# Kernel optimization log

Hardware: AMD Instinct MI355X
Metric: run time of the kernel (lower is better)

The kernel has to match this reference:

```python
import jax, jax.numpy as jnp
import numpy as np

D_MODEL, D_STATE, D_CONV, EXPAND = 1024, 16, 4, 2
D_INNER = EXPAND * D_MODEL
BATCH, SEQLEN = 2, 1024


def setup_inputs() -> dict:
    key = jax.random.key(0)
    ks = jax.random.split(key, 8)
    s = lambda fan: 1.0 / np.sqrt(fan)
    x = jax.random.normal(ks[0], (BATCH, SEQLEN, D_MODEL), jnp.float32)
    in_proj_w = jax.random.normal(ks[1], (2 * D_INNER, D_MODEL), jnp.float32) * s(D_MODEL)
    conv_w = jax.random.normal(ks[2], (D_INNER, D_CONV), jnp.float32) * s(D_CONV)
    conv_b = jax.random.normal(ks[3], (D_INNER,), jnp.float32) * 0.02
    x_proj_w = jax.random.normal(ks[4], (2 * D_STATE + 1, D_INNER), jnp.float32) * s(D_INNER)
    dt_proj_w = jax.random.normal(ks[5], (D_INNER, 1), jnp.float32)
    dt_proj_b = jax.random.normal(ks[6], (D_INNER,), jnp.float32) * 0.02
    A_log = jnp.log(jnp.broadcast_to(jnp.arange(1, D_STATE + 1, dtype=jnp.float32), (D_INNER, D_STATE)))
    D_param = jnp.ones((D_INNER,), jnp.float32)
    out_proj_w = jax.random.normal(ks[7], (D_MODEL, D_INNER), jnp.float32) * s(D_INNER)
    return {"x": x, "in_proj_w": in_proj_w, "conv_w": conv_w, "conv_b": conv_b,
            "x_proj_w": x_proj_w, "dt_proj_w": dt_proj_w, "dt_proj_b": dt_proj_b,
            "A_log": A_log, "D_param": D_param, "out_proj_w": out_proj_w}


def reference(x, in_proj_w, conv_w, conv_b, x_proj_w, dt_proj_w, dt_proj_b, A_log, D_param, out_proj_w):
    B, L, _ = x.shape
    d_inner, d_conv = conv_w.shape
    N = A_log.shape[1]

    # in_proj: [B,L,d_model] -> [B,L,2*d_inner], split into ssm branch and gate
    xz = x @ in_proj_w.T
    x_ssm, z = jnp.split(xz, 2, axis=-1)

    # causal depthwise conv1d (padding d_conv-1 on the left, truncated to L)
    xpad = jnp.pad(x_ssm, ((0, 0), (d_conv - 1, 0), (0, 0)))
    xc = conv_b + sum(conv_w[:, k] * xpad[:, k:k + L, :] for k in range(d_conv))
    xc = jax.nn.silu(xc)

    # selective SSM
    A = -jnp.exp(A_log)                                    # [d_inner, N]
    xp = xc @ x_proj_w.T                                   # [B,L,2N+1]
    dt_r, Bv, Cv = xp[..., :1], xp[..., 1:1 + N], xp[..., 1 + N:]
    dt = jax.nn.softplus(dt_r @ dt_proj_w.T + dt_proj_b)   # [B,L,d_inner]
    dA = jnp.exp(dt[..., None] * A)                        # [B,L,d_inner,N]
    dBx = (dt * xc)[..., None] * Bv[:, :, None, :]         # [B,L,d_inner,N]

    def step(h, inputs):
        dA_t, dBx_t, C_t = inputs                          # [B,D,N],[B,D,N],[B,N]
        h = dA_t * h + dBx_t
        y = jnp.einsum('bdn,bn->bd', h, C_t)
        return h, y

    h0 = jnp.zeros((B, d_inner, N), x.dtype)
    xs = (jnp.moveaxis(dA, 1, 0), jnp.moveaxis(dBx, 1, 0), jnp.moveaxis(Cv, 1, 0))
    _, ys = jax.lax.scan(step, h0, xs)                     # ys: [L,B,d_inner]
    y = jnp.moveaxis(ys, 0, 1) + xc * D_param

    y = y * jax.nn.silu(z)
    return y @ out_proj_w.T
```

## Files before the change

kernel.cpp:

```cpp
#include <hip/hip_runtime.h>
#include <hip/hip_bf16.h>
#include <math.h>

#define B_   2
#define L_   1024
#define DM   1024
#define DI   2048
#define NS   16
#define NPJ  33
#define XPW_STRIDE 64
#define NCH  32
#define CHL  32

typedef __bf16 bf16x8 __attribute__((ext_vector_type(8)));
typedef float  f32x4  __attribute__((ext_vector_type(4)));

__device__ __forceinline__ unsigned short f2bf_rn(float x) {
    union { float f; unsigned u; } a; a.f = x;
    unsigned r = a.u + 0x7fffu + ((a.u >> 16) & 1u);
    return (unsigned short)(r >> 16);
}
__device__ __forceinline__ float bf2f(unsigned short h) {
    union { unsigned u; float f; } a; a.u = ((unsigned)h) << 16;
    return a.f;
}
__device__ __forceinline__ float sigmoidf_(float x) { return 1.f / (1.f + __expf(-x)); }
__device__ __forceinline__ float softplusf_(float x) {
    return x > 20.f ? x : log1pf(__expf(x));
}

#define GLDS(g, l) __builtin_amdgcn_global_load_lds( \
    (__attribute__((address_space(1))) void*)(g),    \
    (__attribute__((address_space(3))) void*)(l), 16, 0, 0)

__global__ __launch_bounds__(256) void cast_hilo_kernel(
    const float* __restrict__ in, unsigned short* __restrict__ hi,
    unsigned short* __restrict__ lo, int n4)
{
    int i = blockIdx.x * 256 + threadIdx.x;
    if (i >= n4) return;
    float4 v = ((const float4*)in)[i];
    ushort4 H, L;
    H.x = f2bf_rn(v.x); L.x = f2bf_rn(v.x - bf2f(H.x));
    H.y = f2bf_rn(v.y); L.y = f2bf_rn(v.y - bf2f(H.y));
    H.z = f2bf_rn(v.z); L.z = f2bf_rn(v.z - bf2f(H.z));
    H.w = f2bf_rn(v.w); L.w = f2bf_rn(v.w - bf2f(H.w));
    ((ushort4*)hi)[i] = H;
    ((ushort4*)lo)[i] = L;
}

__global__ __launch_bounds__(256) void cast_pad_w_kernel(
    const float* __restrict__ W, unsigned short* __restrict__ wh,
    unsigned short* __restrict__ wl)
{
    int i = blockIdx.x * 256 + threadIdx.x;
    int j = i >> 9;
    float4 v = make_float4(0.f, 0.f, 0.f, 0.f);
    if (j < NPJ) v = ((const float4*)W)[i];
    ushort4 H, L;
    H.x = f2bf_rn(v.x); L.x = f2bf_rn(v.x - bf2f(H.x));
    H.y = f2bf_rn(v.y); L.y = f2bf_rn(v.y - bf2f(H.y));
    H.z = f2bf_rn(v.z); L.z = f2bf_rn(v.z - bf2f(H.z));
    H.w = f2bf_rn(v.w); L.w = f2bf_rn(v.w - bf2f(H.w));
    ((ushort4*)wh)[i] = H;
    ((ushort4*)wl)[i] = L;
}

template<int BM, int BN, bool AL>
__global__ __launch_bounds__(256) void gemm3_bt(
    const unsigned short* __restrict__ Ah, const unsigned short* __restrict__ Al,
    const unsigned short* __restrict__ Bh, const unsigned short* __restrict__ Bl,
    float* __restrict__ C, int M, int N, int K, int KC)
{
    constexpr int BK = 64;
    constexpr int FM = BM / 32;
    constexpr int FN = BN / 32;
    __shared__ alignas(16) char sAh[BM * BK * 2];
    __shared__ alignas(16) char sAl[AL ? BM * BK * 2 : 16];
    __shared__ alignas(16) char sBh[BN * BK * 2];
    __shared__ alignas(16) char sBl[BN * BK * 2];

    const int tid  = threadIdx.x;
    const int lane = tid & 63;
    const int wave = tid >> 6;
    const int wm = wave >> 1, wn = wave & 1;
    const int m0 = blockIdx.y * BM, n0 = blockIdx.x * BN;
    const int k0 = blockIdx.z * KC;

    f32x4 acc[FM][FN];
#pragma unroll
    for (int i = 0; i < FM; ++i)
#pragma unroll
        for (int j = 0; j < FN; ++j)
            acc[i][j] = (f32x4){0.f, 0.f, 0.f, 0.f};

    for (int kt = k0; kt < k0 + KC; kt += BK) {
#pragma unroll
        for (int iss = 0; iss < BM / 32; ++iss) {
            int o  = (iss * 256 + tid) * 16;
            int r  = o >> 7;
            int cb = (o & 127) ^ ((r & 7) << 4);
            size_t goff = (size_t)(m0 + r) * K + kt + (cb >> 1);
            GLDS(Ah + goff, sAh + iss * 4096 + wave * 1024);
            if (AL) GLDS(Al + goff, sAl + iss * 4096 + wave * 1024);
        }
#pragma unroll
        for (int iss = 0; iss < BN / 32; ++iss) {
            int o  = (iss * 256 + tid) * 16;
            int r  = o >> 7;
            int cb = (o & 127) ^ ((r & 7) << 4);
            size_t goff = (size_t)(n0 + r) * K + kt + (cb >> 1);
            GLDS(Bh + goff, sBh + iss * 4096 + wave * 1024);
            GLDS(Bl + goff, sBl + iss * 4096 + wave * 1024);
        }
        __syncthreads();

#pragma unroll
        for (int kk = 0; kk < 2; ++kk) {
            const int ke = kk * 32 + (lane >> 4) * 8;
            bf16x8 ah[FM], al[FM], bh[FN], bl[FN];
#pragma unroll
            for (int i = 0; i < FM; ++i) {
                int r = wm * (BM / 2) + i * 16 + (lane & 15);
                int off = (r * 128 + ke * 2) ^ ((r & 7) << 4);
                ah[i] = *(const bf16x8*)(sAh + off);
                if (AL) al[i] = *(const bf16x8*)(sAl + off);
            }
#pragma unroll
            for (int j = 0; j < FN; ++j) {
                int r = wn * (BN / 2) + j * 16 + (lane & 15);
                int off = (r * 128 + ke * 2) ^ ((r & 7) << 4);
                bh[j] = *(const bf16x8*)(sBh + off);
                bl[j] = *(const bf16x8*)(sBl + off);
            }
#pragma unroll
            for (int i = 0; i < FM; ++i)
#pragma unroll
                for (int j = 0; j < FN; ++j) {
                    acc[i][j] = __builtin_amdgcn_mfma_f32_16x16x32_bf16(ah[i], bh[j], acc[i][j], 0, 0, 0);
                    acc[i][j] = __builtin_amdgcn_mfma_f32_16x16x32_bf16(ah[i], bl[j], acc[i][j], 0, 0, 0);
                    if (AL) acc[i][j] = __builtin_amdgcn_mfma_f32_16x16x32_bf16(al[i], bh[j], acc[i][j], 0, 0, 0);
                }
        }
        __syncthreads();
    }

    float* Cz = C + (size_t)blockIdx.z * M * N;
#pragma unroll
    for (int i = 0; i < FM; ++i)
#pragma unroll
        for (int j = 0; j < FN; ++j) {
            int row = m0 + wm * (BM / 2) + i * 16 + (lane >> 4) * 4;
            int col = n0 + wn * (BN / 2) + j * 16 + (lane & 15);
            float* p = Cz + (size_t)row * N + col;
#pragma unroll
            for (int q = 0; q < 4; ++q) p[(size_t)q * N] = acc[i][j][q];
        }
}

__global__ __launch_bounds__(256) void reduce4_kernel(
    const float* __restrict__ part, float* __restrict__ out, int n4, int stride4)
{
    int i = blockIdx.x * 256 + threadIdx.x;
    if (i >= n4) return;
    const float4* p = (const float4*)part;
    float4 s = p[i];
#pragma unroll
    for (int z = 1; z < 4; ++z) {
        float4 v = p[(size_t)z * stride4 + i];
        s.x += v.x; s.y += v.y; s.z += v.z; s.w += v.w;
    }
    ((float4*)out)[i] = s;
}

__global__ __launch_bounds__(256) void gemm3_xproj(
    const unsigned short* __restrict__ Ah, const unsigned short* __restrict__ Al,
    const unsigned short* __restrict__ Bh, const unsigned short* __restrict__ Bl,
    float* __restrict__ part)
{
    constexpr int BM = 64, BN = 64, BK = 64, KTOT = 2048, KC = 256;
    __shared__ alignas(16) char sAh[BM * 128];
    __shared__ alignas(16) char sAl[BM * 128];
    __shared__ alignas(16) char sBh[BN * 128];
    __shared__ alignas(16) char sBl[BN * 128];

    const int tid  = threadIdx.x;
    const int lane = tid & 63;
    const int wave = tid >> 6;
    const int wm = wave >> 1, wn = wave & 1;
    const int m0 = blockIdx.y * BM;
    const int kt0 = blockIdx.z * KC;

    f32x4 acc[2][2];
#pragma unroll
    for (int i = 0; i < 2; ++i)
#pragma unroll
        for (int j = 0; j < 2; ++j) acc[i][j] = (f32x4){0.f, 0.f, 0.f, 0.f};

    for (int kt = 0; kt < KC; kt += BK) {
#pragma unroll
        for (int iss = 0; iss < 2; ++iss) {
            int o  = (iss * 256 + tid) * 16;
            int r  = o >> 7;
            int cb = (o & 127) ^ ((r & 7) << 4);
            size_t ga = (size_t)(m0 + r) * KTOT + kt0 + kt + (cb >> 1);
            GLDS(Ah + ga, sAh + iss * 4096 + wave * 1024);
            GLDS(Al + ga, sAl + iss * 4096 + wave * 1024);
            size_t gb = (size_t)r * KTOT + kt0 + kt + (cb >> 1);
            GLDS(Bh + gb, sBh + iss * 4096 + wave * 1024);
            GLDS(Bl + gb, sBl + iss * 4096 + wave * 1024);
        }
        __syncthreads();

#pragma unroll
        for (int kk = 0; kk < 2; ++kk) {
            const int ke = kk * 32 + (lane >> 4) * 8;
            bf16x8 ah[2], al[2], bh[2], bl[2];
#pragma unroll
            for (int i = 0; i < 2; ++i) {
                int r = wm * 32 + i * 16 + (lane & 15);
                int off = (r * 128 + ke * 2) ^ ((r & 7) << 4);
                ah[i] = *(const bf16x8*)(sAh + off);
                al[i] = *(const bf16x8*)(sAl + off);
            }
#pragma unroll
            for (int j = 0; j < 2; ++j) {
                int r = wn * 32 + j * 16 + (lane & 15);
                int off = (r * 128 + ke * 2) ^ ((r & 7) << 4);
                bh[j] = *(const bf16x8*)(sBh + off);
                bl[j] = *(const bf16x8*)(sBl + off);
            }
#pragma unroll
            for (int i = 0; i < 2; ++i)
#pragma unroll
                for (int j = 0; j < 2; ++j) {
                    acc[i][j] = __builtin_amdgcn_mfma_f32_16x16x32_bf16(ah[i], bh[j], acc[i][j], 0, 0, 0);
                    acc[i][j] = __builtin_amdgcn_mfma_f32_16x16x32_bf16(ah[i], bl[j], acc[i][j], 0, 0, 0);
                    acc[i][j] = __builtin_amdgcn_mfma_f32_16x16x32_bf16(al[i], bh[j], acc[i][j], 0, 0, 0);
                }
        }
        __syncthreads();
    }

    float* Cp = part + (size_t)blockIdx.z * 2048 * XPW_STRIDE;
#pragma unroll
    for (int i = 0; i < 2; ++i)
#pragma unroll
        for (int j = 0; j < 2; ++j) {
            int row = m0 + wm * 32 + i * 16 + (lane >> 4) * 4;
            int col = wn * 32 + j * 16 + (lane & 15);
            float* p = Cp + (size_t)row * XPW_STRIDE + col;
#pragma unroll
            for (int q = 0; q < 4; ++q) p[(size_t)q * XPW_STRIDE] = acc[i][j][q];
        }
}

__global__ __launch_bounds__(256) void xproj_reduce(
    const float* __restrict__ part, float* __restrict__ xp)
{
    int i = blockIdx.x * 256 + threadIdx.x;
    const float4* p = (const float4*)part;
    float4 s = p[i];
#pragma unroll
    for (int z = 1; z < 8; ++z) {
        float4 v = p[(size_t)z * 32768 + i];
        s.x += v.x; s.y += v.y; s.z += v.z; s.w += v.w;
    }
    ((float4*)xp)[i] = s;
}

__global__ __launch_bounds__(256) void conv_silu_kernel(
    const float* __restrict__ xz, const float* __restrict__ cw,
    const float* __restrict__ cb, unsigned short* __restrict__ xch,
    unsigned short* __restrict__ xcl)
{
    int gid = blockIdx.x * 256 + threadIdx.x;
    int m  = gid >> 9;
    int dv = (gid & 511) << 2;
    int t  = m & (L_ - 1);
    const float* base = xz + (size_t)m * (2 * DI) + dv;
    float4 s  = *(const float4*)(cb + dv);
    float4 w0 = *(const float4*)(cw + (dv + 0) * 4);
    float4 w1 = *(const float4*)(cw + (dv + 1) * 4);
    float4 w2 = *(const float4*)(cw + (dv + 2) * 4);
    float4 w3 = *(const float4*)(cw + (dv + 3) * 4);
    float4 z4 = make_float4(0.f, 0.f, 0.f, 0.f);
    float4 x3 = *(const float4*)(base);
    float4 x2 = (t >= 1) ? *(const float4*)(base - 1 * (2 * DI)) : z4;
    float4 x1 = (t >= 2) ? *(const float4*)(base - 2 * (2 * DI)) : z4;
    float4 x0 = (t >= 3) ? *(const float4*)(base - 3 * (2 * DI)) : z4;
    float r0 = s.x + w0.x * x0.x + w0.y * x1.x + w0.z * x2.x + w0.w * x3.x;
    float r1 = s.y + w1.x * x0.y + w1.y * x1.y + w1.z * x2.y + w1.w * x3.y;
    float r2 = s.z + w2.x * x0.z + w2.y * x1.z + w2.z * x2.z + w2.w * x3.z;
    float r3 = s.w + w3.x * x0.w + w3.y * x1.w + w3.z * x2.w + w3.w * x3.w;
    float4 o;
    o.x = r0 * sigmoidf_(r0);
    o.y = r1 * sigmoidf_(r1);
    o.z = r2 * sigmoidf_(r2);
    o.w = r3 * sigmoidf_(r3);
    ushort4 H, L;
    H.x = f2bf_rn(o.x); L.x = f2bf_rn(o.x - bf2f(H.x));
    H.y = f2bf_rn(o.y); L.y = f2bf_rn(o.y - bf2f(H.y));
    H.z = f2bf_rn(o.z); L.z = f2bf_rn(o.z - bf2f(H.z));
    H.w = f2bf_rn(o.w); L.w = f2bf_rn(o.w - bf2f(H.w));
    *(ushort4*)(xch + (size_t)m * DI + dv) = H;
    *(ushort4*)(xcl + (size_t)m * DI + dv) = L;
}

__global__ __launch_bounds__(256) void scan_pass1(
    const unsigned short* __restrict__ xch, const unsigned short* __restrict__ xcl,
    const float* __restrict__ xp,
    const float* __restrict__ dtw, const float* __restrict__ dtb,
    const float* __restrict__ A_log, float* __restrict__ h0, float* __restrict__ sumdt)
{
    const int b = blockIdx.z, c = blockIdx.y;
    const int tid = threadIdx.x;
    const int d = blockIdx.x * 256 + tid;
    __shared__ float sxp[CHL * XPW_STRIDE];
    const float* xpsrc = xp + (size_t)(b * L_ + c * CHL) * XPW_STRIDE;
    for (int i = tid; i < CHL * XPW_STRIDE / 4; i += 256)
        ((float4*)sxp)[i] = ((const float4*)xpsrc)[i];
    __syncthreads();

    float Av[NS];
#pragma unroll
    for (int n = 0; n < NS; ++n) Av[n] = -__expf(A_log[(size_t)d * NS + n]);
    const float w = dtw[d], bb = dtb[d];
    float h[NS];
#pragma unroll
    for (int n = 0; n < NS; ++n) h[n] = 0.f;
    float sd = 0.f;
    size_t off = (size_t)(b * L_ + c * CHL) * DI + d;

    unsigned short nh = xch[off], nl = xcl[off];
    for (int t = 0; t < CHL; ++t) {
        unsigned short ch = nh, cl = nl;
        nh = xch[off + DI]; nl = xcl[off + DI];
        off += DI;
        float xcv = bf2f(ch) + bf2f(cl);
        float dt  = softplusf_(fmaf(sxp[t * XPW_STRIDE], w, bb));
        sd += dt;
        float u = dt * xcv;
#pragma unroll
        for (int n = 0; n < NS; ++n) {
            float a = __expf(dt * Av[n]);
            h[n] = fmaf(a, h[n], u * sxp[t * XPW_STRIDE + 1 + n]);
        }
    }
    float* hp = h0 + ((size_t)(b * NCH + c) * DI + d) * NS;
#pragma unroll
    for (int n = 0; n < NS; n += 4)
        *(float4*)(hp + n) = make_float4(h[n], h[n + 1], h[n + 2], h[n + 3]);
    sumdt[(size_t)(b * NCH + c) * DI + d] = sd;
}

__global__ __launch_bounds__(256) void scan_pass2(
    const float* __restrict__ A_log, const float* __restrict__ sumdt, float* __restrict__ h0)
{
    int gid = blockIdx.x * 256 + threadIdx.x;
    int b = gid >> 15;
    int r = gid & 32767;
    int d = r >> 4, n = r & 15;
    float An = -__expf(A_log[(size_t)d * NS + n]);
    float h = 0.f;
    for (int c = 0; c < NCH; ++c) {
        size_t idx = ((size_t)(b * NCH + c) * DI + d) * NS + n;
        float hl  = h0[idx];
        float sdv = sumdt[(size_t)(b * NCH + c) * DI + d];
        h0[idx] = h;
        h = fmaf(__expf(An * sdv), h, hl);
    }
}

__global__ __launch_bounds__(256) void scan_pass3(
    const unsigned short* __restrict__ xch, const unsigned short* __restrict__ xcl,
    const float* __restrict__ xp, const float* __restrict__ xz,
    const float* __restrict__ dtw, const float* __restrict__ dtb,
    const float* __restrict__ A_log, const float* __restrict__ Dp,
    const float* __restrict__ hin,
    unsigned short* __restrict__ yh)
{
    const int b = blockIdx.z, c = blockIdx.y;
    const int tid = threadIdx.x;
    const int d = blockIdx.x * 256 + tid;
    __shared__ float sxp[CHL * XPW_STRIDE];
    const float* xpsrc = xp + (size_t)(b * L_ + c * CHL) * XPW_STRIDE;
    for (int i = tid; i < CHL * XPW_STRIDE / 4; i += 256)
        ((float4*)sxp)[i] = ((const float4*)xpsrc)[i];
    __syncthreads();

    float Av[NS];
#pragma unroll
    for (int n = 0; n < NS; ++n) Av[n] = -__expf(A_log[(size_t)d * NS + n]);
    const float w = dtw[d], bb = dtb[d], Dv = Dp[d];
    float h[NS];
    const float* hp = hin + ((size_t)(b * NCH + c) * DI + d) * NS;
#pragma unroll
    for (int n = 0; n < NS; n += 4) {
        float4 v = *(const float4*)(hp + n);
        h[n] = v.x; h[n + 1] = v.y; h[n + 2] = v.z; h[n + 3] = v.w;
    }
    size_t off = (size_t)(b * L_ + c * CHL) * DI + d;
    const float* zp  = xz + (size_t)(b * L_ + c * CHL) * (2 * DI) + DI + d;
    unsigned short* yhp = yh + off;

    unsigned short nh = xch[off], nl = xcl[off];
    float nz = zp[0];
    for (int t = 0; t < CHL; ++t) {
        unsigned short ch = nh, cl = nl;
        float zv = nz;
        nh = xch[off + DI]; nl = xcl[off + DI];
        nz = zp[(size_t)(t + 1) * (2 * DI)];
        off += DI;
        float xcv = bf2f(ch) + bf2f(cl);
        float dt  = softplusf_(fmaf(sxp[t * XPW_STRIDE], w, bb));
        float u = dt * xcv;
        float y = 0.f;
#pragma unroll
        for (int n = 0; n < NS; ++n) {
            float a = __expf(dt * Av[n]);
            h[n] = fmaf(a, h[n], u * sxp[t * XPW_STRIDE + 1 + n]);
            y = fmaf(h[n], sxp[t * XPW_STRIDE + 17 + n], y);
        }
        float out = fmaf(xcv, Dv, y) * (zv * sigmoidf_(zv));
        yhp[(size_t)t * DI] = f2bf_rn(out);
    }
}

extern "C" void kernel_launch(void* const* d_in, const int* in_sizes, int n_in,
                              void* d_out, int out_size, void* d_ws, size_t ws_size,
                              hipStream_t stream)
{
    (void)in_sizes; (void)n_in; (void)out_size;
    const float* x    = (const float*)d_in[0];
    const float* w1   = (const float*)d_in[1];
    const float* cw   = (const float*)d_in[2];
    const float* cb   = (const float*)d_in[3];
    const float* xpw  = (const float*)d_in[4];
    const float* dtw  = (const float*)d_in[5];
    const float* dtb  = (const float*)d_in[6];
    const float* alog = (const float*)d_in[7];
    const float* Dp   = (const float*)d_in[8];
    const float* w2   = (const float*)d_in[9];
    float* out = (float*)d_out;

    char* ws = (char*)d_ws;
    const size_t MB = 1024 * 1024;
    const size_t KB = 1024;
    if (ws_size < 81 * MB) return;

    unsigned short* x_hi  = (unsigned short*)(ws + 0);
    unsigned short* x_lo  = (unsigned short*)(ws + 4 * MB);
    unsigned short* w1_hi = (unsigned short*)(ws + 8 * MB);
    unsigned short* w1_lo = (unsigned short*)(ws + 16 * MB);
    float* xp_part = (float*)(ws + 16 * MB);
    unsigned short* y_hi  = (unsigned short*)(ws + 0);
    float* h0    = (float*)(ws + 8 * MB);
    float* sumdt = (float*)(ws + 16 * MB);
    float* xz = (float*)(ws + 24 * MB);
    float* c_part = (float*)(ws + 24 * MB);
    unsigned short* xc_hi = (unsigned short*)(ws + 56 * MB);
    unsigned short* xc_lo = (unsigned short*)(ws + 64 * MB);
    float* xp = (float*)(ws + 72 * MB);
    unsigned short* wp_hi = (unsigned short*)(ws + 72 * MB + 512 * KB);
    unsigned short* wp_lo = (unsigned short*)(ws + 72 * MB + 768 * KB);
    unsigned short* w2_hi = (unsigned short*)(ws + 73 * MB);
    unsigned short* w2_lo = (unsigned short*)(ws + 77 * MB);

    cast_hilo_kernel<<<(2 * 1024 * 1024 / 4) / 256, 256, 0, stream>>>(x, x_hi, x_lo, 2 * 1024 * 1024 / 4);
    cast_hilo_kernel<<<(4 * 1024 * 1024 / 4) / 256, 256, 0, stream>>>(w1, w1_hi, w1_lo, 4 * 1024 * 1024 / 4);
    cast_hilo_kernel<<<(2 * 1024 * 1024 / 4) / 256, 256, 0, stream>>>(w2, w2_hi, w2_lo, 2 * 1024 * 1024 / 4);
    cast_pad_w_kernel<<<128, 256, 0, stream>>>(xpw, wp_hi, wp_lo);

    {
        dim3 g(4096 / 128, 2048 / 128, 1);
        gemm3_bt<128, 128, true><<<g, 256, 0, stream>>>(x_hi, x_lo, w1_hi, w1_lo, xz, 2048, 4096, 1024, 1024);
    }

    conv_silu_kernel<<<(2048 * 512) / 256, 256, 0, stream>>>(xz, cw, cb, xc_hi, xc_lo);

    {
        dim3 g(1, 2048 / 64, 8);
        gemm3_xproj<<<g, 256, 0, stream>>>(xc_hi, xc_lo, wp_hi, wp_lo, xp_part);
        xproj_reduce<<<128, 256, 0, stream>>>(xp_part, xp);
    }

    {
        dim3 gs(DI / 256, NCH, B_);
        scan_pass1<<<gs, 256, 0, stream>>>(xc_hi, xc_lo, xp, dtw, dtb, alog, h0, sumdt);
        scan_pass2<<<(B_ * DI * NS) / 256, 256, 0, stream>>>(alog, sumdt, h0);
        scan_pass3<<<gs, 256, 0, stream>>>(xc_hi, xc_lo, xp, xz, dtw, dtb, alog, Dp, h0, y_hi);
    }

    {
        dim3 g(1024 / 128, 2048 / 128, 4);
        gemm3_bt<128, 128, false><<<g, 256, 0, stream>>>(y_hi, nullptr, w2_hi, w2_lo, c_part, 2048, 1024, 2048, 512);
        reduce4_kernel<<<(2048 * 1024 / 4 + 255) / 256, 256, 0, stream>>>(c_part, out, 2048 * 1024 / 4, 2048 * 1024 / 4);
    }
}
```

Measured before the change: 190.3 us.

## Merge cast kernels, use atomic split-K for out_proj, double scan chunks

Fuses the four fp32-to-bf16 hi/lo cast launches into one kernel and replaces the split-K partial buffer plus reduce kernel with a memset and atomicAdd epilogue written directly into the output. It also changes the chunked scan from 32 chunks of 32 steps to 64 chunks of 16, and moves the sumdt scratch into the output buffer. This cuts launches and the partial-sum traffic and gives the scan more parallelism. The cost is fp32 atomic contention and nondeterministic summation order, plus a longer sequential pass2 across chunks.

```diff
diff --git a/kernel.cpp b/kernel.cpp
--- a/kernel.cpp
+++ b/kernel.cpp
@@ -9,8 +9,8 @@
 #define NS   16
 #define NPJ  33
 #define XPW_STRIDE 64
-#define NCH  32
-#define CHL  32
+#define NCH  64
+#define CHL  16
 
 typedef __bf16 bf16x8 __attribute__((ext_vector_type(8)));
 typedef float  f32x4  __attribute__((ext_vector_type(4)));
@@ -33,40 +33,46 @@
     (__attribute__((address_space(1))) void*)(g),    \
     (__attribute__((address_space(3))) void*)(l), 16, 0, 0)
 
-__global__ __launch_bounds__(256) void cast_hilo_kernel(
-    const float* __restrict__ in, unsigned short* __restrict__ hi,
-    unsigned short* __restrict__ lo, int n4)
+#define XN4   524288
+#define W1N4  1048576
+#define W2N4  524288
+#define WPN4  32768
+__global__ __launch_bounds__(256) void cast_all_kernel(
+    const float* __restrict__ x, const float* __restrict__ w1,
+    const float* __restrict__ w2, const float* __restrict__ xpw,
+    unsigned short* __restrict__ xh, unsigned short* __restrict__ xl,
+    unsigned short* __restrict__ w1h, unsigned short* __restrict__ w1l,
+    unsigned short* __restrict__ w2h, unsigned short* __restrict__ w2l,
+    unsigned short* __restrict__ wph, unsigned short* __restrict__ wpl)
 {
     int i = blockIdx.x * 256 + threadIdx.x;
-    if (i >= n4) return;
-    float4 v = ((const float4*)in)[i];
+    float4 v;
+    ushort4 *dh, *dl;
+    int li;
+    if (i < XN4) {
+        li = i; v = ((const float4*)x)[li];
+        dh = (ushort4*)xh; dl = (ushort4*)xl;
+    } else if (i < XN4 + W1N4) {
+        li = i - XN4; v = ((const float4*)w1)[li];
+        dh = (ushort4*)w1h; dl = (ushort4*)w1l;
+    } else if (i < XN4 + W1N4 + W2N4) {
+        li = i - (XN4 + W1N4); v = ((const float4*)w2)[li];
+        dh = (ushort4*)w2h; dl = (ushort4*)w2l;
+    } else if (i < XN4 + W1N4 + W2N4 + WPN4) {
+        li = i - (XN4 + W1N4 + W2N4);
+        int j = li >> 9;
+        v = (j < NPJ) ? ((const float4*)xpw)[li] : make_float4(0.f, 0.f, 0.f, 0.f);
+        dh = (ushort4*)wph; dl = (ushort4*)wpl;
+    } else return;
     ushort4 H, L;
     H.x = f2bf_rn(v.x); L.x = f2bf_rn(v.x - bf2f(H.x));
     H.y = f2bf_rn(v.y); L.y = f2bf_rn(v.y - bf2f(H.y));
     H.z = f2bf_rn(v.z); L.z = f2bf_rn(v.z - bf2f(H.z));
     H.w = f2bf_rn(v.w); L.w = f2bf_rn(v.w - bf2f(H.w));
-    ((ushort4*)hi)[i] = H;
-    ((ushort4*)lo)[i] = L;
-}
-
-__global__ __launch_bounds__(256) void cast_pad_w_kernel(
-    const float* __restrict__ W, unsigned short* __restrict__ wh,
-    unsigned short* __restrict__ wl)
-{
-    int i = blockIdx.x * 256 + threadIdx.x;
-    int j = i >> 9;
-    float4 v = make_float4(0.f, 0.f, 0.f, 0.f);
-    if (j < NPJ) v = ((const float4*)W)[i];
-    ushort4 H, L;
-    H.x = f2bf_rn(v.x); L.x = f2bf_rn(v.x - bf2f(H.x));
-    H.y = f2bf_rn(v.y); L.y = f2bf_rn(v.y - bf2f(H.y));
-    H.z = f2bf_rn(v.z); L.z = f2bf_rn(v.z - bf2f(H.z));
-    H.w = f2bf_rn(v.w); L.w = f2bf_rn(v.w - bf2f(H.w));
-    ((ushort4*)wh)[i] = H;
-    ((ushort4*)wl)[i] = L;
-}
-
-template<int BM, int BN, bool AL>
+    dh[li] = H; dl[li] = L;
+}
+
+template<int BM, int BN, bool AL, bool ATOMIC>
 __global__ __launch_bounds__(256) void gemm3_bt(
     const unsigned short* __restrict__ Ah, const unsigned short* __restrict__ Al,
     const unsigned short* __restrict__ Bh, const unsigned short* __restrict__ Bl,
@@ -145,7 +151,7 @@
         __syncthreads();
     }
 
-    float* Cz = C + (size_t)blockIdx.z * M * N;
+    float* Cz = ATOMIC ? C : (C + (size_t)blockIdx.z * M * N);
 #pragma unroll
     for (int i = 0; i < FM; ++i)
 #pragma unroll
@@ -154,23 +160,11 @@
             int col = n0 + wn * (BN / 2) + j * 16 + (lane & 15);
             float* p = Cz + (size_t)row * N + col;
 #pragma unroll
-            for (int q = 0; q < 4; ++q) p[(size_t)q * N] = acc[i][j][q];
-        }
-}
-
-__global__ __launch_bounds__(256) void reduce4_kernel(
-    const float* __restrict__ part, float* __restrict__ out, int n4, int stride4)
-{
-    int i = blockIdx.x * 256 + threadIdx.x;
-    if (i >= n4) return;
-    const float4* p = (const float4*)part;
-    float4 s = p[i];
-#pragma unroll
-    for (int z = 1; z < 4; ++z) {
-        float4 v = p[(size_t)z * stride4 + i];
-        s.x += v.x; s.y += v.y; s.z += v.z; s.w += v.w;
-    }
-    ((float4*)out)[i] = s;
+            for (int q = 0; q < 4; ++q) {
+                if (ATOMIC) atomicAdd(p + (size_t)q * N, acc[i][j][q]);
+                else        p[(size_t)q * N] = acc[i][j][q];
+            }
+        }
 }
 
 __global__ __launch_bounds__(256) void gemm3_xproj(
@@ -456,9 +450,8 @@
     float* xp_part = (float*)(ws + 16 * MB);
     unsigned short* y_hi  = (unsigned short*)(ws + 0);
     float* h0    = (float*)(ws + 8 * MB);
-    float* sumdt = (float*)(ws + 16 * MB);
+    float* sumdt = (float*)d_out;
     float* xz = (float*)(ws + 24 * MB);
-    float* c_part = (float*)(ws + 24 * MB);
     unsigned short* xc_hi = (unsigned short*)(ws + 56 * MB);
     unsigned short* xc_lo = (unsigned short*)(ws + 64 * MB);
     float* xp = (float*)(ws + 72 * MB);
@@ -467,14 +460,15 @@
     unsigned short* w2_hi = (unsigned short*)(ws + 73 * MB);
     unsigned short* w2_lo = (unsigned short*)(ws + 77 * MB);
 
-    cast_hilo_kernel<<<(2 * 1024 * 1024 / 4) / 256, 256, 0, stream>>>(x, x_hi, x_lo, 2 * 1024 * 1024 / 4);
-    cast_hilo_kernel<<<(4 * 1024 * 1024 / 4) / 256, 256, 0, stream>>>(w1, w1_hi, w1_lo, 4 * 1024 * 1024 / 4);
-    cast_hilo_kernel<<<(2 * 1024 * 1024 / 4) / 256, 256, 0, stream>>>(w2, w2_hi, w2_lo, 2 * 1024 * 1024 / 4);
-    cast_pad_w_kernel<<<128, 256, 0, stream>>>(xpw, wp_hi, wp_lo);
+    {
+        int total = XN4 + W1N4 + W2N4 + WPN4;
+        cast_all_kernel<<<(total + 255) / 256, 256, 0, stream>>>(
+            x, w1, w2, xpw, x_hi, x_lo, w1_hi, w1_lo, w2_hi, w2_lo, wp_hi, wp_lo);
+    }
 
     {
         dim3 g(4096 / 128, 2048 / 128, 1);
-        gemm3_bt<128, 128, true><<<g, 256, 0, stream>>>(x_hi, x_lo, w1_hi, w1_lo, xz, 2048, 4096, 1024, 1024);
+        gemm3_bt<128, 128, true, false><<<g, 256, 0, stream>>>(x_hi, x_lo, w1_hi, w1_lo, xz, 2048, 4096, 1024, 1024);
     }
 
     conv_silu_kernel<<<(2048 * 512) / 256, 256, 0, stream>>>(xz, cw, cb, xc_hi, xc_lo);
@@ -493,8 +487,8 @@
     }
 
     {
+        hipMemsetAsync(out, 0, (size_t)2048 * 1024 * 4, stream);
         dim3 g(1024 / 128, 2048 / 128, 4);
-        gemm3_bt<128, 128, false><<<g, 256, 0, stream>>>(y_hi, nullptr, w2_hi, w2_lo, c_part, 2048, 1024, 2048, 512);
-        reduce4_kernel<<<(2048 * 1024 / 4 + 255) / 256, 256, 0, stream>>>(c_part, out, 2048 * 1024 / 4, 2048 * 1024 / 4);
-    }
-}
+        gemm3_bt<128, 128, false, true><<<g, 256, 0, stream>>>(y_hi, nullptr, w2_hi, w2_lo, out, 2048, 1024, 2048, 512);
+    }
+}
```

Result: slower. 201.7 us (+6.0%).
